# Kernel optimization log

Measured on AMD Instinct MI355X. Metric: run time of the kernel, lower is better.

The kernel has to match this reference:

```python
import jax, jax.numpy as jnp
import numpy as np

B, L, D = 2, 4096, 2048
H = 8
DK = D // H   # head qk dim = 256
DV = D // H   # head v dim = 256
KCONV = 4
BT = 64       # chunk size
EPS = 1e-5


def setup_inputs() -> dict:
    key = jax.random.key(0)
    ks = jax.random.split(key, 10)
    s = 0.02  # xavier-ish init scale (gain 2**-2.5)
    return {
        "hidden_states": jax.random.normal(ks[0], (B, L, D), jnp.float32),
        "Wq": jax.random.normal(ks[1], (D, D), jnp.float32) * s,
        "Wk": jax.random.normal(ks[2], (D, D), jnp.float32) * s,
        "Wv": jax.random.normal(ks[3], (D, D), jnp.float32) * s,
        "Wb": jax.random.normal(ks[4], (H, D), jnp.float32) * s,
        "conv_q": jax.random.normal(ks[5], (D, KCONV), jnp.float32) * 0.5,
        "conv_k": jax.random.normal(ks[6], (D, KCONV), jnp.float32) * 0.5,
        "conv_v": jax.random.normal(ks[7], (D, KCONV), jnp.float32) * 0.5,
        "g_norm": jnp.ones((DV,), jnp.float32),
        "Wo": jax.random.normal(ks[8], (D, D), jnp.float32) * s,
    }


def _causal_conv_silu(x, w):
    # depthwise causal conv1d (ShortConvolution), x: [B,L,C], w: [C,K]; silu activation
    K = w.shape[1]
    xp = jnp.pad(x, ((0, 0), (K - 1, 0), (0, 0)))
    Lx = x.shape[1]
    y = xp[:, 0:Lx, :] * w[:, 0]
    for j in range(1, K):
        y = y + xp[:, j:j + Lx, :] * w[:, j]
    return jax.nn.silu(y)


def _l2norm(x):
    return x * jax.lax.rsqrt(jnp.sum(x * x, -1, keepdims=True) + 1e-6)


def _chunk_delta_rule(q, k, v, beta):
    # q,k: [B,H,L,DK], v: [B,H,L,DV], beta: [B,H,L]
    b, h, Lq, dk = q.shape
    dv = v.shape[-1]
    nc = Lq // BT
    q = q * (dk ** -0.5)
    kb = k * beta[..., None]
    vb = v * beta[..., None]
    ch = lambda x: x.reshape(b, h, nc, BT, x.shape[-1])
    qc, kc, kbc, vbc = ch(q), ch(k), ch(kb), ch(vb)
    tri_s = jnp.tril(jnp.ones((BT, BT), bool), -1)  # strictly lower
    tri = jnp.tril(jnp.ones((BT, BT), bool))        # lower incl diag
    # M = strict_lower(K_beta K^T); T = (I+M)^{-1} via unit-lower triangular solve
    M = jnp.where(tri_s, jnp.einsum('bhntd,bhnsd->bhnts', kbc, kc), 0.0)
    Lmat = jnp.eye(BT, dtype=q.dtype) + M
    W = jax.scipy.linalg.solve_triangular(Lmat, kbc, lower=True, unit_diagonal=True)  # T @ k_beta
    U = jax.scipy.linalg.solve_triangular(Lmat, vbc, lower=True, unit_diagonal=True)  # T @ v_beta

    def step(S, xs):
        q_i, k_i, w_i, u_i = xs  # each [b,h,BT,d]
        attn = jnp.where(tri, jnp.einsum('bhtd,bhsd->bhts', q_i, k_i), 0.0)
        u_new = u_i - jnp.einsum('bhtd,bhdv->bhtv', w_i, S)
        o_i = jnp.einsum('bhtd,bhdv->bhtv', q_i, S) + jnp.einsum('bhts,bhsv->bhtv', attn, u_new)
        S = S + jnp.einsum('bhtd,bhtv->bhdv', k_i, u_new)
        return S, o_i

    mv = lambda x: jnp.moveaxis(x, 2, 0)  # chunk axis to front for scan
    S0 = jnp.zeros((b, h, dk, dv), q.dtype)
    S, o = jax.lax.scan(step, S0, (mv(qc), mv(kc), mv(W), mv(U)))
    o = jnp.moveaxis(o, 0, 2).reshape(b, h, Lq, dv)
    return o, S


def reference(hidden_states, Wq, Wk, Wv, Wb, conv_q, conv_k, conv_v, g_norm, Wo):
    hs = hidden_states
    q = _causal_conv_silu(hs @ Wq.T, conv_q)
    k = _causal_conv_silu(hs @ Wk.T, conv_k)
    v = _causal_conv_silu(hs @ Wv.T, conv_v)
    tohead = lambda x: x.reshape(B, L, H, -1).transpose(0, 2, 1, 3)  # b l (h d) -> b h l d
    q, k, v = tohead(q), tohead(k), tohead(v)
    q, k = _l2norm(q), _l2norm(k)
    beta = jax.nn.sigmoid(hs @ Wb.T).transpose(0, 2, 1)  # [B,H,L]
    o, _ = _chunk_delta_rule(q, k, v, beta)
    o = o.transpose(0, 2, 1, 3)  # [B,L,H,DV]
    o = o * jax.lax.rsqrt(jnp.mean(o * o, -1, keepdims=True) + EPS) * g_norm  # per-head RMSNorm
    return o.reshape(B, L, D) @ Wo.T
```

## Files before the change

kernel.cpp:

```cpp
#include <hip/hip_runtime.h>
#include <stdint.h>

#define TOK    8192
#define LDIM   4096
#define DDIM   2048
#define NBH    16
#define DK     256
#define NCHUNK 64
#define DVS    16

typedef __attribute__((ext_vector_type(8))) short bf16x8;
typedef __attribute__((ext_vector_type(4))) float f32x4;

#define MFMA(a,b,c) __builtin_amdgcn_mfma_f32_16x16x32_bf16((a),(b),(c),0,0,0)

__device__ __forceinline__ unsigned short f2bf(float f){
  union { float f; uint32_t u; } v; v.f = f;
  uint32_t r = v.u + 0x7FFFu + ((v.u >> 16) & 1u);
  return (unsigned short)(r >> 16);
}
__device__ __forceinline__ float bf2f(unsigned short u){
  union { uint32_t u; float f; } v; v.u = ((uint32_t)u) << 16;
  return v.f;
}

typedef __attribute__((address_space(1))) unsigned int as1_u32;
typedef __attribute__((address_space(3))) unsigned int as3_u32;
__device__ __forceinline__ void gload16(const void* g, void* l){
  __builtin_amdgcn_global_load_lds((const as1_u32*)g, (as3_u32*)l, 16, 0, 0);
}

__device__ __forceinline__ void bar_lds(){
  asm volatile("s_waitcnt lgkmcnt(0)\n\ts_barrier" ::: "memory");
}

__global__ void k_guard(float* o){ if (threadIdx.x == 0) o[0] = 0.f; }

__global__ __launch_bounds__(256) void k_f2bf(const float* __restrict__ s,
                                              unsigned short* __restrict__ d, int n)
{
  int i = (blockIdx.x*256 + threadIdx.x)*4;
  if (i >= n) return;
  float4 v = *(const float4*)(s + i);
  ushort4 o; o.x=f2bf(v.x); o.y=f2bf(v.y); o.z=f2bf(v.z); o.w=f2bf(v.w);
  *(ushort4*)(d + i) = o;
}

__global__ __launch_bounds__(256) void k_beta(const float* __restrict__ hs,
                                              const float* __restrict__ Wb,
                                              float* __restrict__ beta,
                                              unsigned short* __restrict__ hsb)
{
  const long t = blockIdx.x;
  const int tid = threadIdx.x;
  float acc[8] = {0,0,0,0,0,0,0,0};
  const float* xr = hs + t*DDIM;
  unsigned short* hb = hsb + t*DDIM;
  for (int i = tid; i < DDIM; i += 256){
    float x = xr[i];
    hb[i] = f2bf(x);
    #pragma unroll
    for (int h=0; h<8; h++) acc[h] += x * Wb[h*DDIM + i];
  }
  __shared__ float red[8][4];
  const int w = tid >> 6, lane = tid & 63;
  #pragma unroll
  for (int h=0; h<8; h++){
    float s = acc[h];
    #pragma unroll
    for (int off=32; off; off>>=1) s += __shfl_down(s, off, 64);
    if (lane == 0) red[h][w] = s;
  }
  __syncthreads();
  if (tid < 8){
    float s = red[tid][0]+red[tid][1]+red[tid][2]+red[tid][3];
    float bv = 1.f/(1.f + __expf(-s));
    int b = (int)(t >> 12), l = (int)(t & 4095);
    beta[((long)(b*8 + tid))*LDIM + l] = bv;
  }
}

template <bool F32OUT>
__global__ __launch_bounds__(512) void k_gemm256(
    const unsigned short* __restrict__ A, const unsigned short* __restrict__ Bw,
    void* __restrict__ Cv, int M, int N, int K)
{
  __shared__ unsigned short As[4][256*32];
  __shared__ unsigned short Bs[4][256*32];
  const int tid = threadIdx.x;
  const int w = tid >> 6, l = tid & 63;
  const int lo = l & 15, quad = l >> 4;
  const int wm = w >> 2, wn = w & 3;
  const int gx = gridDim.x;
  int id = blockIdx.y * gx + blockIdx.x;
  const int nwg = gx * gridDim.y;
  if ((nwg & 7) == 0){ const int q8 = nwg >> 3; id = (id & 7)*q8 + (id >> 3); }
  const int bx = id % gx, by = id / gx;
  const long tm = (long)by * 256, tn = (long)bx * 256;

  const int slot0 = (w*2+0)*64 + l;
  const int slot1 = (w*2+1)*64 + l;
  const int r0 = slot0 >> 2, c0 = ((slot0 & 3)*16) ^ (((r0 >> 1) & 3) << 4);
  const int r1 = slot1 >> 2, c1 = ((slot1 & 3)*16) ^ (((r1 >> 1) & 3) << 4);
  const unsigned short* pA0 = A  + (tm + r0)*(long)K + (c0 >> 1);
  const unsigned short* pA1 = A  + (tm + r1)*(long)K + (c1 >> 1);
  const unsigned short* pB0 = Bw + (tn + r0)*(long)K + (c0 >> 1);
  const unsigned short* pB1 = Bw + (tn + r1)*(long)K + (c1 >> 1);
  const int asw = ((quad*16) ^ (((lo >> 1) & 3) << 4)) >> 1;

  f32x4 acc[8][4] = {};
  const int nt = K >> 5;

#define STAGE(t_) do { const int kk_ = (t_)*32, b_ = (t_) & 3;      \
    gload16(pA0 + kk_, &As[b_][slot0*8]);                           \
    gload16(pA1 + kk_, &As[b_][slot1*8]);                           \
    gload16(pB0 + kk_, &Bs[b_][slot0*8]);                           \
    gload16(pB1 + kk_, &Bs[b_][slot1*8]); } while(0)

#define COMPUTE(t_) do { const int b_ = (t_) & 3;                              \
    bf16x8 af[8], bg[4];                                                       \
    _Pragma("unroll")                                                          \
    for (int mf=0; mf<8; mf++)                                                 \
      af[mf] = *(const bf16x8*)&As[b_][(wm*128 + mf*16 + lo)*32 + asw];        \
    _Pragma("unroll")                                                          \
    for (int nf=0; nf<4; nf++)                                                 \
      bg[nf] = *(const bf16x8*)&Bs[b_][(wn*64 + nf*16 + lo)*32 + asw];         \
    _Pragma("unroll")                                                          \
    for (int mf=0; mf<8; mf++)                                                 \
      _Pragma("unroll")                                                        \
      for (int nf=0; nf<4; nf++)                                               \
        acc[mf][nf] = MFMA(af[mf], bg[nf], acc[mf][nf]); } while(0)

  STAGE(0); STAGE(1);
  #pragma unroll 1
  for (int t = 0; t < nt-2; ++t){
    STAGE(t+2);
    asm volatile("s_waitcnt vmcnt(8)" ::: "memory");
    bar_lds();
    COMPUTE(t);
  }
  asm volatile("s_waitcnt vmcnt(4)" ::: "memory");
  bar_lds();
  COMPUTE(nt-2);
  asm volatile("s_waitcnt vmcnt(0)" ::: "memory");
  bar_lds();
  COMPUTE(nt-1);
#undef STAGE
#undef COMPUTE

  #pragma unroll
  for (int mf=0; mf<8; mf++)
    #pragma unroll
    for (int nf=0; nf<4; nf++)
      #pragma unroll
      for (int r=0; r<4; r++){
        long m = tm + wm*128 + mf*16 + quad*4 + r;
        long n = tn + wn*64 + nf*16 + lo;
        if (F32OUT) ((float*)Cv)[m*N + n] = acc[mf][nf][r];
        else ((unsigned short*)Cv)[m*N + n] = f2bf(acc[mf][nf][r]);
      }
}

__global__ __launch_bounds__(256) void k_conv(
  const unsigned short* __restrict__ X, const float* __restrict__ Wc,
  const float* __restrict__ beta,
  unsigned short* __restrict__ O, int mode)
{
  const int lt = blockIdx.x, bh = blockIdx.y;
  const int b = bh >> 3, h = bh & 7;
  const int d = threadIdx.x;
  const int ch = h*256 + d;
  const int l0 = lt*64;
  const unsigned short* xp = X + (long)b*LDIM*DDIM + ch;
  const float4 wv = *(const float4*)(Wc + ch*4);
  float x0=0.f, x1=0.f, x2=0.f;
  if (l0 >= 3){
    x0 = bf2f(xp[(long)(l0-3)*DDIM]);
    x1 = bf2f(xp[(long)(l0-2)*DDIM]);
    x2 = bf2f(xp[(long)(l0-1)*DDIM]);
  }
  float y[64];
  #pragma unroll
  for (int i=0;i<64;i++){
    float x3 = bf2f(xp[(long)(l0+i)*DDIM]);
    float s = x0*wv.x + x1*wv.y + x2*wv.z + x3*wv.w;
    y[i] = s / (1.f + __expf(-s));
    x0 = x1; x1 = x2; x2 = x3;
  }
  unsigned short* op = O + (long)bh*LDIM*DK + d;
  if (mode == 2){
    const float* bet = beta + (long)bh*LDIM + l0;
    #pragma unroll
    for (int i=0;i<64;i++) op[(long)(l0+i)*DK] = f2bf(y[i]*bet[i]);
    return;
  }
  __shared__ float red[64*4];
  __shared__ float scl[64];
  const int wv_i = threadIdx.x >> 6, lane = threadIdx.x & 63;
  #pragma unroll
  for (int i=0;i<64;i++){
    float ss = y[i]*y[i];
    #pragma unroll
    for (int off=32; off; off>>=1) ss += __shfl_down(ss, off, 64);
    if (lane == 0) red[i*4 + wv_i] = ss;
  }
  __syncthreads();
  if (threadIdx.x < 64){
    int i = threadIdx.x;
    float s = red[i*4]+red[i*4+1]+red[i*4+2]+red[i*4+3];
    scl[i] = rsqrtf(s + 1e-6f) * (mode==0 ? 0.0625f : 1.f);
  }
  __syncthreads();
  #pragma unroll
  for (int i=0;i<64;i++) op[(long)(l0+i)*DK] = f2bf(y[i]*scl[i]);
}

__global__ __launch_bounds__(256) void k_transpose(
  const unsigned short* __restrict__ kH, unsigned short* __restrict__ kT)
{
  const int lt = blockIdx.x, dt = blockIdx.y, bh = blockIdx.z;
  __shared__ unsigned short tk[64][72];
  const int tid = threadIdx.x;
  const int rl = tid >> 2, c0 = (tid & 3) * 16;
  const long base = ((long)bh*LDIM + lt*64 + rl)*DK + dt*64 + c0;
  *(bf16x8*)&tk[rl][c0]   = *(const bf16x8*)(kH + base);
  *(bf16x8*)&tk[rl][c0+8] = *(const bf16x8*)(kH + base + 8);
  __syncthreads();
  const int rd = tid >> 2, lc0 = (tid & 3) * 16;
  bf16x8 ok0, ok1;
  #pragma unroll
  for (int j=0;j<16;j++){
    unsigned short kraw = tk[lc0+j][rd];
    if (j < 8) ok0[j] = (short)kraw; else ok1[j-8] = (short)kraw;
  }
  const long ob = (((long)bh*NCHUNK + lt)*DK + dt*64 + rd)*64 + lc0;
  *(bf16x8*)(kT + ob) = ok0; *(bf16x8*)(kT + ob + 8) = ok1;
}

__global__ __launch_bounds__(256) void k_passA(
  const unsigned short* __restrict__ qH, const unsigned short* __restrict__ kH,
  const unsigned short* vbH,
  const unsigned short* __restrict__ kT,
  const float* __restrict__ beta,
  unsigned short* Wout,
  unsigned short* __restrict__ Uout,
  unsigned short* __restrict__ Aout)
{
  const int c = blockIdx.x, bh = blockIdx.y;
  __shared__ unsigned short Nn[64*72];
  __shared__ unsigned short NT[64*72];
  __shared__ unsigned short Pb[64*72];
  __shared__ unsigned short vT[256*72];
  const int tid = threadIdx.x;
  const int w = tid >> 6, l = tid & 63, lo = l & 15, quad = l >> 4;
  const long tokBase = (long)bh*LDIM + c*64;
  const unsigned short* qrow = qH + tokBase*DK;
  const unsigned short* krow = kH + tokBase*DK;
  const float bv = beta[tokBase + w*16 + lo];

  {
    const int r = tid >> 2, cs = (tid & 3) * 64;
    const unsigned short* vrow = vbH + (tokBase + r)*DK + cs;
    bf16x8 vv[8];
    #pragma unroll
    for (int j=0;j<8;j++) vv[j] = *(const bf16x8*)(vrow + j*8);
    #pragma unroll
    for (int j=0;j<8;j++)
      #pragma unroll
      for (int e=0;e<8;e++)
        vT[(cs + j*8 + e)*72 + r] = (unsigned short)vv[j][e];
  }

  f32x4 mAcc[4] = {}; f32x4 aAcc[4] = {};
  #pragma unroll
  for (int ks=0; ks<8; ks++){
    bf16x8 kf[4];
    #pragma unroll
    for (int nt=0; nt<4; nt++)
      kf[nt] = *(const bf16x8*)&krow[(nt*16+lo)*DK + ks*32 + quad*8];
    bf16x8 qf  = *(const bf16x8*)&qrow[(w*16+lo)*DK + ks*32 + quad*8];
    bf16x8 kfw = *(const bf16x8*)&krow[(w*16+lo)*DK + ks*32 + quad*8];
    bf16x8 kbf;
    #pragma unroll
    for (int j=0;j<8;j++) kbf[j] = (short)f2bf(bf2f((unsigned short)kfw[j]) * bv);
    #pragma unroll
    for (int nt=0; nt<4; nt++){
      mAcc[nt] = MFMA(kbf, kf[nt], mAcc[nt]);
      aAcc[nt] = MFMA(qf,  kf[nt], aAcc[nt]);
    }
  }
  unsigned short* Ap = Aout + ((long)bh*NCHUNK + c)*64*64;
  #pragma unroll
  for (int nt=0; nt<4; nt++)
    #pragma unroll
    for (int r=0; r<4; r++){
      int t = w*16 + quad*4 + r, s = nt*16 + lo;
      float mv = (t > s) ? mAcc[nt][r] : 0.f;
      unsigned short mb = f2bf(mv);
      Nn[t*72+s] = mb;
      NT[s*72+t] = mb;
      Pb[t*72+s] = f2bf((t==s ? 1.f : 0.f) - mv);
      Ap[t*64+s] = f2bf((t >= s) ? aAcc[nt][r] : 0.f);
    }
  __syncthreads();

  #pragma unroll 1
  for (int it=0; it<5; it++){
    bf16x8 aN[2], aP[2], bN[2][4];
    #pragma unroll
    for (int ks=0; ks<2; ks++){
      aN[ks] = *(const bf16x8*)&Nn[(w*16+lo)*72 + ks*32 + quad*8];
      aP[ks] = *(const bf16x8*)&Pb[(w*16+lo)*72 + ks*32 + quad*8];
      #pragma unroll
      for (int nt=0; nt<4; nt++)
        bN[ks][nt] = *(const bf16x8*)&NT[(nt*16+lo)*72 + ks*32 + quad*8];
    }
    f32x4 pp[4];
    #pragma unroll
    for (int nt=0; nt<4; nt++)
      #pragma unroll
      for (int r=0; r<4; r++)
        pp[nt][r] = bf2f(Pb[(w*16+quad*4+r)*72 + nt*16+lo]);
    __syncthreads();
    f32x4 sq[4] = {};
    #pragma unroll
    for (int ks=0; ks<2; ks++)
      #pragma unroll
      for (int nt=0; nt<4; nt++)
        sq[nt] = MFMA(aN[ks], bN[ks][nt], sq[nt]);
    #pragma unroll
    for (int nt=0; nt<4; nt++)
      #pragma unroll
      for (int r=0; r<4; r++){
        int t = w*16 + quad*4 + r, s = nt*16 + lo;
        unsigned short vb2 = f2bf(sq[nt][r]);
        Nn[t*72+s] = vb2; NT[s*72+t] = vb2;
      }
    __syncthreads();
    #pragma unroll
    for (int ks=0; ks<2; ks++)
      #pragma unroll
      for (int nt=0; nt<4; nt++){
        bf16x8 b = *(const bf16x8*)&NT[(nt*16+lo)*72 + ks*32 + quad*8];
        pp[nt] = MFMA(aP[ks], b, pp[nt]);
      }
    #pragma unroll
    for (int nt=0; nt<4; nt++)
      #pragma unroll
      for (int r=0; r<4; r++)
        Pb[(w*16+quad*4+r)*72 + nt*16+lo] = f2bf(pp[nt][r]);
    __syncthreads();
  }

  float b8[2][8];
  #pragma unroll
  for (int ks=0; ks<2; ks++)
    #pragma unroll
    for (int e=0; e<8; e++)
      b8[ks][e] = beta[tokBase + ks*32 + quad*8 + e];
  const unsigned short* kTb = kT + ((long)bh*NCHUNK + c)*DK*64;
  unsigned short* Wp = Wout + tokBase*DK;
  unsigned short* Up = Uout + tokBase*DK;
  #pragma unroll 1
  for (int nl=0; nl<4; nl++){
    const int d = (w*4 + nl)*16 + lo;
    f32x4 wa[4] = {}; f32x4 ua[4] = {};
    #pragma unroll
    for (int ks=0; ks<2; ks++){
      bf16x8 braw = *(const bf16x8*)&kTb[(long)d*64 + ks*32 + quad*8];
      bf16x8 bw;
      #pragma unroll
      for (int e=0; e<8; e++) bw[e] = (short)f2bf(bf2f((unsigned short)braw[e]) * b8[ks][e]);
      bf16x8 bu = *(const bf16x8*)&vT[d*72 + ks*32 + quad*8];
      #pragma unroll
      for (int mt=0; mt<4; mt++){
        bf16x8 a = *(const bf16x8*)&Pb[(mt*16+lo)*72 + ks*32 + quad*8];
        wa[mt] = MFMA(a, bw, wa[mt]);
        ua[mt] = MFMA(a, bu, ua[mt]);
      }
    }
    #pragma unroll
    for (int mt=0; mt<4; mt++)
      #pragma unroll
      for (int r=0; r<4; r++){
        int t = mt*16 + quad*4 + r;
        Wp[t*DK + d] = f2bf(wa[mt][r]);
        Up[t*DK + d] = f2bf(ua[mt][r]);
      }
  }
}

__device__ __forceinline__ int sidx(int n, int d){
  return n*256 + (((d>>3) ^ (n&7))<<3) + (d&7);
}
__device__ __forceinline__ int uidx(int n, int t){
  return n*64 + ((((t>>3) ^ (n&7)) & 7)<<3) + (t&7);
}

struct PrefWU {
  bf16x8 wf[8];
  unsigned short uf[4];
};

__device__ __forceinline__ void load_wu(PrefWU& P,
    const unsigned short* __restrict__ Wp, const unsigned short* __restrict__ Up,
    int c, int w, int lo, int quad, int vb)
{
  const unsigned short* Wc = Wp + (long)c*64*DK;
  const unsigned short* Uc = Up + (long)c*64*DK;
  #pragma unroll
  for (int ks=0; ks<8; ks++)
    P.wf[ks] = *(const bf16x8*)&Wc[(w*16+lo)*DK + ks*32 + quad*8];
  const int t0 = w*16 + quad*4;
  #pragma unroll
  for (int r=0; r<4; r++)
    P.uf[r] = Uc[(t0+r)*DK + vb*DVS + lo];
}

__device__ __forceinline__ void scan_chunk(PrefWU& P, int c, int cnext,
  const unsigned short* __restrict__ Wp, const unsigned short* __restrict__ Up,
  const unsigned short* __restrict__ qp, const unsigned short* __restrict__ kTp,
  const unsigned short* __restrict__ Ap, unsigned short* __restrict__ op,
  const unsigned short* __restrict__ Srd, unsigned short* __restrict__ Swr,
  unsigned short* __restrict__ u_l, f32x4 (&S)[4],
  int w, int lo, int quad, int vb)
{
  const unsigned short* qc = qp + (long)c*64*DK;
  const unsigned short* Ac = Ap + (long)c*64*64;
  const unsigned short* kc = kTp + (long)c*DK*64;
  const int t0 = w*16 + quad*4;
  bf16x8 qf[8], af[2];
  #pragma unroll
  for (int ks=0; ks<8; ks++)
    qf[ks] = *(const bf16x8*)&qc[(w*16+lo)*DK + ks*32 + quad*8];
  #pragma unroll
  for (int ks=0; ks<2; ks++)
    af[ks] = *(const bf16x8*)&Ac[(w*16+lo)*64 + ks*32 + quad*8];

  bf16x8 sb[8];
  #pragma unroll
  for (int ks=0; ks<8; ks++)
    sb[ks] = *(const bf16x8*)&Srd[sidx(lo, ks*32+quad*8)];
  f32x4 ua0 = {}, ua1 = {};
  #pragma unroll
  for (int ks=0; ks<4; ks++){
    ua0 = MFMA(P.wf[ks],   sb[ks],   ua0);
    ua1 = MFMA(P.wf[ks+4], sb[ks+4], ua1);
  }
  {
    ushort4 pk;
    pk.x = f2bf(bf2f(P.uf[0]) - (ua0[0]+ua1[0]));
    pk.y = f2bf(bf2f(P.uf[1]) - (ua0[1]+ua1[1]));
    pk.z = f2bf(bf2f(P.uf[2]) - (ua0[2]+ua1[2]));
    pk.w = f2bf(bf2f(P.uf[3]) - (ua0[3]+ua1[3]));
    *(ushort4*)&u_l[uidx(lo, t0)] = pk;
  }
  __syncthreads();

  load_wu(P, Wp, Up, cnext, w, lo, quad, vb);
  bf16x8 kf[4][2];
  #pragma unroll
  for (int mtl=0; mtl<4; mtl++)
    #pragma unroll
    for (int ks=0; ks<2; ks++)
      kf[mtl][ks] = *(const bf16x8*)&kc[(w*64+mtl*16+lo)*64 + ks*32 + quad*8];

  f32x4 oa0 = {}, oa1 = {};
  #pragma unroll
  for (int ks=0; ks<4; ks++){
    oa0 = MFMA(qf[ks],   sb[ks],   oa0);
    oa1 = MFMA(qf[ks+4], sb[ks+4], oa1);
  }
  bf16x8 ub[2];
  #pragma unroll
  for (int ks=0; ks<2; ks++)
    ub[ks] = *(const bf16x8*)&u_l[uidx(lo, ks*32+quad*8)];
  #pragma unroll
  for (int ks=0; ks<2; ks++)
    oa0 = MFMA(af[ks], ub[ks], oa0);
  #pragma unroll
  for (int r=0; r<4; r++)
    op[(long)(c*64 + t0 + r)*DK + vb*DVS + lo] = f2bf(oa0[r] + oa1[r]);

  #pragma unroll
  for (int mtl=0; mtl<4; mtl++)
    #pragma unroll
    for (int ks=0; ks<2; ks++)
      S[mtl] = MFMA(kf[mtl][ks], ub[ks], S[mtl]);
  #pragma unroll
  for (int mtl=0; mtl<4; mtl++){
    const int d0 = w*64 + mtl*16 + quad*4;
    ushort4 pk;
    pk.x = f2bf(S[mtl][0]); pk.y = f2bf(S[mtl][1]);
    pk.z = f2bf(S[mtl][2]); pk.w = f2bf(S[mtl][3]);
    *(ushort4*)&Swr[sidx(lo, d0)] = pk;
  }
  __syncthreads();
}

__global__ __launch_bounds__(256,1) void k_scan(
  const unsigned short* __restrict__ Wm, const unsigned short* __restrict__ Um,
  const unsigned short* __restrict__ qH, const unsigned short* __restrict__ kT,
  const unsigned short* __restrict__ Abuf, unsigned short* __restrict__ oH)
{
  const int bh = blockIdx.x, vb = blockIdx.y;
  __shared__ unsigned short S_l[2][DVS*256];
  __shared__ unsigned short u_l[DVS*64];
  const int tid = threadIdx.x;
  const int w = tid >> 6, l = tid & 63, lo = l & 15, quad = l >> 4;
  for (int i = tid; i < DVS*256/4; i += 256) ((unsigned long long*)S_l[0])[i] = 0ULL;
  f32x4 S[4] = {};
  const long hb = (long)bh * LDIM;
  const unsigned short* Wp = Wm + hb*DK;
  const unsigned short* Up = Um + hb*DK;
  const unsigned short* qp = qH + hb*DK;
  const unsigned short* kTp = kT + (long)bh*NCHUNK*DK*64;
  const unsigned short* Ap = Abuf + (long)bh*NCHUNK*64*64;
  unsigned short* op = oH + hb*DK;
  PrefWU P;
  load_wu(P, Wp, Up, 0, w, lo, quad, vb);
  __syncthreads();
  #pragma unroll 1
  for (int c = 0; c < NCHUNK; c += 2){
    scan_chunk(P, c,   c+1, Wp, Up, qp, kTp, Ap, op, S_l[0], S_l[1], u_l, S, w, lo, quad, vb);
    scan_chunk(P, c+1, (c+2 < NCHUNK) ? c+2 : NCHUNK-1,
               Wp, Up, qp, kTp, Ap, op, S_l[1], S_l[0], u_l, S, w, lo, quad, vb);
  }
}

__global__ __launch_bounds__(64) void k_rms(
  const unsigned short* __restrict__ oH, const float* __restrict__ g,
  unsigned short* __restrict__ oN)
{
  const int ln = blockIdx.x, bh = blockIdx.y;
  const int b = bh >> 3, h = bh & 7;
  ushort4 u = *(const ushort4*)(oH + ((long)bh*LDIM + ln)*DK + threadIdx.x*4);
  float4 v; v.x = bf2f(u.x); v.y = bf2f(u.y); v.z = bf2f(u.z); v.w = bf2f(u.w);
  float ss = v.x*v.x + v.y*v.y + v.z*v.z + v.w*v.w;
  #pragma unroll
  for (int off=32; off; off>>=1) ss += __shfl_down(ss, off, 64);
  ss = __shfl(ss, 0, 64);
  const float sc = rsqrtf(ss*(1.f/DK) + 1e-5f);
  const float4 gv = *(const float4*)(g + threadIdx.x*4);
  unsigned short* o = oN + ((long)b*LDIM + ln)*DDIM + h*DK + threadIdx.x*4;
  ushort4 pk; pk.x=f2bf(v.x*sc*gv.x); pk.y=f2bf(v.y*sc*gv.y);
  pk.z=f2bf(v.z*sc*gv.z); pk.w=f2bf(v.w*sc*gv.w);
  *(ushort4*)o = pk;
}

extern "C" void kernel_launch(void* const* d_in, const int* in_sizes, int n_in,
                              void* d_out, int out_size, void* d_ws, size_t ws_size,
                              hipStream_t stream)
{
  (void)in_sizes; (void)n_in; (void)out_size;
  const float* hs = (const float*)d_in[0];
  const float* Wq = (const float*)d_in[1];
  const float* Wk = (const float*)d_in[2];
  const float* Wv = (const float*)d_in[3];
  const float* Wb = (const float*)d_in[4];
  const float* cq = (const float*)d_in[5];
  const float* ck = (const float*)d_in[6];
  const float* cv = (const float*)d_in[7];
  const float* gn = (const float*)d_in[8];
  const float* Wo = (const float*)d_in[9];

  const size_t SZ_TD2 = (size_t)TOK*DDIM*2;
  const size_t SZ_DD2 = (size_t)DDIM*DDIM*2;
  const size_t NEED  = 5*SZ_TD2 + 2*SZ_DD2 + (size_t)NBH*LDIM*4;
  const size_t NEEDW = NEED + SZ_TD2;
  if (ws_size < NEED){ k_guard<<<1, 64, 0, stream>>>((float*)d_out); return; }

  char* p = (char*)d_ws;
  unsigned short* bufA = (unsigned short*)p;      p += SZ_TD2;
  unsigned short* bufB = (unsigned short*)p;      p += SZ_DD2;
  unsigned short* bufC = (unsigned short*)p;      p += SZ_TD2;
  unsigned short* bufD = (unsigned short*)p;      p += SZ_TD2;
  unsigned short* bufE = (unsigned short*)p;      p += SZ_TD2;
  unsigned short* bufF = (unsigned short*)p;      p += SZ_TD2;
  unsigned short* bufG = (unsigned short*)p;      p += SZ_DD2;
  float*          beta = (float*)p;               p += (size_t)NBH*LDIM*4;
  unsigned short* bufW = (ws_size >= NEEDW) ? (unsigned short*)p : bufF;

  const dim3 gg(DDIM/256, TOK/256);
  const dim3 cg(LDIM/64, NBH);
  const int nDD = DDIM*DDIM;

  k_beta<<<dim3(TOK), 256, 0, stream>>>(hs, Wb, beta, bufA);

  k_f2bf<<<dim3(nDD/1024), 256, 0, stream>>>(Wq, bufB, nDD);
  k_gemm256<false><<<gg, 512, 0, stream>>>(bufA, bufB, bufC, TOK, DDIM, DDIM);
  k_conv<<<cg, 256, 0, stream>>>(bufC, cq, beta, bufD, 0);

  k_f2bf<<<dim3(nDD/1024), 256, 0, stream>>>(Wk, bufB, nDD);
  k_gemm256<false><<<gg, 512, 0, stream>>>(bufA, bufB, bufC, TOK, DDIM, DDIM);
  k_conv<<<cg, 256, 0, stream>>>(bufC, ck, beta, bufE, 1);

  k_f2bf<<<dim3(nDD/1024), 256, 0, stream>>>(Wv, bufB, nDD);
  k_gemm256<false><<<gg, 512, 0, stream>>>(bufA, bufB, bufC, TOK, DDIM, DDIM);
  k_conv<<<cg, 256, 0, stream>>>(bufC, cv, beta, bufF, 2);

  k_transpose<<<dim3(LDIM/64, DK/64, NBH), 256, 0, stream>>>(bufE, bufC);
  k_passA<<<dim3(NCHUNK, NBH), 256, 0, stream>>>(bufD, bufE, bufF, bufC, beta,
                                                 bufW, bufA , bufG);
  k_scan<<<dim3(NBH, 16), 256, 0, stream>>>(bufW, bufA, bufD, bufC, bufG, bufE);
  k_rms<<<dim3(LDIM, NBH), 64, 0, stream>>>(bufE, gn, bufC);

  k_f2bf<<<dim3(nDD/1024), 256, 0, stream>>>(Wo, bufB, nDD);
  k_gemm256<true><<<gg, 512, 0, stream>>>(bufC, bufB, d_out , TOK, DDIM, DDIM);
}
```

Measured before the change: 864.4 us.

## Deepen GEMM K-tile to 64 with double buffering and post-compute staging

Result: no change. 877.6 us (+1.5%).

```diff
diff --git a/kernel.cpp b/kernel.cpp
--- a/kernel.cpp
+++ b/kernel.cpp
@@ -85,8 +85,8 @@
     const unsigned short* __restrict__ A, const unsigned short* __restrict__ Bw,
     void* __restrict__ Cv, int M, int N, int K)
 {
-  __shared__ unsigned short As[4][256*32];
-  __shared__ unsigned short Bs[4][256*32];
+  __shared__ unsigned short As[2][256*64];
+  __shared__ unsigned short Bs[2][256*64];
   const int tid = threadIdx.x;
   const int w = tid >> 6, l = tid & 63;
   const int lo = l & 15, quad = l >> 4;
@@ -98,53 +98,62 @@
   const int bx = id % gx, by = id / gx;
   const long tm = (long)by * 256, tn = (long)bx * 256;
 
-  const int slot0 = (w*2+0)*64 + l;
-  const int slot1 = (w*2+1)*64 + l;
-  const int r0 = slot0 >> 2, c0 = ((slot0 & 3)*16) ^ (((r0 >> 1) & 3) << 4);
-  const int r1 = slot1 >> 2, c1 = ((slot1 & 3)*16) ^ (((r1 >> 1) & 3) << 4);
+  const int s0 = (w*4+0)*64 + l, s1 = (w*4+1)*64 + l;
+  const int s2 = (w*4+2)*64 + l, s3 = (w*4+3)*64 + l;
+  const int r0 = s0 >> 3, c0 = ((s0 & 7)*16) ^ (((r0 >> 1) & 3) << 4);
+  const int r1 = s1 >> 3, c1 = ((s1 & 7)*16) ^ (((r1 >> 1) & 3) << 4);
+  const int r2 = s2 >> 3, c2 = ((s2 & 7)*16) ^ (((r2 >> 1) & 3) << 4);
+  const int r3 = s3 >> 3, c3 = ((s3 & 7)*16) ^ (((r3 >> 1) & 3) << 4);
   const unsigned short* pA0 = A  + (tm + r0)*(long)K + (c0 >> 1);
   const unsigned short* pA1 = A  + (tm + r1)*(long)K + (c1 >> 1);
+  const unsigned short* pA2 = A  + (tm + r2)*(long)K + (c2 >> 1);
+  const unsigned short* pA3 = A  + (tm + r3)*(long)K + (c3 >> 1);
   const unsigned short* pB0 = Bw + (tn + r0)*(long)K + (c0 >> 1);
   const unsigned short* pB1 = Bw + (tn + r1)*(long)K + (c1 >> 1);
-  const int asw = ((quad*16) ^ (((lo >> 1) & 3) << 4)) >> 1;
+  const unsigned short* pB2 = Bw + (tn + r2)*(long)K + (c2 >> 1);
+  const unsigned short* pB3 = Bw + (tn + r3)*(long)K + (c3 >> 1);
 
   f32x4 acc[8][4] = {};
-  const int nt = K >> 5;
-
-#define STAGE(t_) do { const int kk_ = (t_)*32, b_ = (t_) & 3;      \
-    gload16(pA0 + kk_, &As[b_][slot0*8]);                           \
-    gload16(pA1 + kk_, &As[b_][slot1*8]);                           \
-    gload16(pB0 + kk_, &Bs[b_][slot0*8]);                           \
-    gload16(pB1 + kk_, &Bs[b_][slot1*8]); } while(0)
-
-#define COMPUTE(t_) do { const int b_ = (t_) & 3;                              \
-    bf16x8 af[8], bg[4];                                                       \
+  const int nt = K >> 6;
+
+#define STAGE(t_) do { const int kk_ = (t_)*64, b_ = (t_) & 1;      \
+    gload16(pA0 + kk_, &As[b_][s0*8]);                              \
+    gload16(pA1 + kk_, &As[b_][s1*8]);                              \
+    gload16(pA2 + kk_, &As[b_][s2*8]);                              \
+    gload16(pA3 + kk_, &As[b_][s3*8]);                              \
+    gload16(pB0 + kk_, &Bs[b_][s0*8]);                              \
+    gload16(pB1 + kk_, &Bs[b_][s1*8]);                              \
+    gload16(pB2 + kk_, &Bs[b_][s2*8]);                              \
+    gload16(pB3 + kk_, &Bs[b_][s3*8]); } while(0)
+
+#define COMPUTE(t_) do { const int b_ = (t_) & 1;                              \
     _Pragma("unroll")                                                          \
-    for (int mf=0; mf<8; mf++)                                                 \
-      af[mf] = *(const bf16x8*)&As[b_][(wm*128 + mf*16 + lo)*32 + asw];        \
-    _Pragma("unroll")                                                          \
-    for (int nf=0; nf<4; nf++)                                                 \
-      bg[nf] = *(const bf16x8*)&Bs[b_][(wn*64 + nf*16 + lo)*32 + asw];         \
-    _Pragma("unroll")                                                          \
-    for (int mf=0; mf<8; mf++)                                                 \
+    for (int ks=0; ks<2; ks++){                                                \
+      bf16x8 af[8], bg[4];                                                     \
+      const int co = ((ks*64 + quad*16) ^ (((lo >> 1) & 3) << 4)) >> 1;        \
+      _Pragma("unroll")                                                        \
+      for (int mf=0; mf<8; mf++)                                               \
+        af[mf] = *(const bf16x8*)&As[b_][(wm*128 + mf*16 + lo)*64 + co];       \
       _Pragma("unroll")                                                        \
       for (int nf=0; nf<4; nf++)                                               \
-        acc[mf][nf] = MFMA(af[mf], bg[nf], acc[mf][nf]); } while(0)
+        bg[nf] = *(const bf16x8*)&Bs[b_][(wn*64 + nf*16 + lo)*64 + co];        \
+      _Pragma("unroll")                                                        \
+      for (int mf=0; mf<8; mf++)                                               \
+        _Pragma("unroll")                                                      \
+        for (int nf=0; nf<4; nf++)                                             \
+          acc[mf][nf] = MFMA(af[mf], bg[nf], acc[mf][nf]);                     \
+    } } while(0)
 
   STAGE(0); STAGE(1);
   #pragma unroll 1
-  for (int t = 0; t < nt-2; ++t){
-    STAGE(t+2);
-    asm volatile("s_waitcnt vmcnt(8)" ::: "memory");
+  for (int t = 0; t < nt; ++t){
+    if (t < nt-1) asm volatile("s_waitcnt vmcnt(8)" ::: "memory");
+    else          asm volatile("s_waitcnt vmcnt(0)" ::: "memory");
     bar_lds();
     COMPUTE(t);
-  }
-  asm volatile("s_waitcnt vmcnt(4)" ::: "memory");
-  bar_lds();
-  COMPUTE(nt-2);
-  asm volatile("s_waitcnt vmcnt(0)" ::: "memory");
-  bar_lds();
-  COMPUTE(nt-1);
+    bar_lds();
+    if (t+2 < nt) STAGE(t+2);
+  }
 #undef STAGE
 #undef COMPUTE
 
```
